# Kernel tuning notes

Measured on AMD Instinct MI355X. Metric: run time of the kernel, lower is better.

## Reference

```python
import jax, jax.numpy as jnp
import numpy as np

B, D_IN, D_DENSE, S1, S2 = 16384, 1024, 1024, 1024, 1024
SPARSITY1, SPARSITY2 = 0.1, 0.01  # fraction of zeros in the 'sparse' weights


def setup_inputs() -> dict:
    key = jax.random.key(0)
    kx, k0, k1, k2, km1, km2 = jax.random.split(key, 6)
    x = jax.random.normal(kx, (B, D_IN), dtype=jnp.float32)
    # dense layer params (nn.Linear): weight [out, in], bias [out]
    w0 = jax.random.normal(k0, (D_DENSE, D_IN), dtype=jnp.float32) / np.sqrt(D_IN)
    b0 = jnp.zeros((D_DENSE,), dtype=jnp.float32)
    # sparse layers: dense randn weight elementwise-masked (mask keeps with prob 1-sparsity)
    w1 = jax.random.normal(k1, (S1, D_DENSE), dtype=jnp.float32)
    mask1 = jax.random.uniform(km1, (S1, D_DENSE)) > SPARSITY1
    b1 = jnp.zeros((S1,), dtype=jnp.float32)
    w2 = jax.random.normal(k2, (S2, S1), dtype=jnp.float32)
    mask2 = jax.random.uniform(km2, (S2, S1)) > SPARSITY2
    b2 = jnp.zeros((S2,), dtype=jnp.float32)
    return {"x": x, "w0": w0, "b0": b0, "w1": w1, "b1": b1, "mask1": mask1,
            "w2": w2, "b2": b2, "mask2": mask2}


def reference(x, w0, b0, w1, b1, mask1, w2, b2, mask2):
    # layer 1: dense linear + ReLU
    h = jax.nn.relu(jnp.einsum('bi,oi->bo', x, w0) + b0)
    # layer 2: masked ('sparse' COO in torch) linear + bias + ReLU
    h = jax.nn.relu(jnp.einsum('bi,oi->bo', h, w1 * mask1) + b1)
    # layer 3: masked linear + bias + ReLU
    out = jax.nn.relu(jnp.einsum('bi,oi->bo', h, w2 * mask2) + b2)
    return out
```

## Files before the change

kernel.cpp:

```cpp
#include <hip/hip_runtime.h>
#include <hip/hip_bf16.h>
#include <cstdint>
#include <cstddef>


typedef __bf16 bf16x8 __attribute__((ext_vector_type(8)));
typedef float  f32x4  __attribute__((ext_vector_type(4)));

#define AS1 __attribute__((address_space(1)))
#define AS3 __attribute__((address_space(3)))

__device__ __forceinline__ void gload_lds16(const void* g, void* l) {
    __builtin_amdgcn_global_load_lds((const AS1 void*)g, (AS3 void*)l, 16, 0, 0);
}

__global__ void detect_mask(const unsigned char* __restrict__ m, int* __restrict__ flag) {
    const int t = threadIdx.x;
    int or1 = 0, or3 = 0;
    for (int e = t; e < 256; e += 64) { or1 |= m[e * 4 + 1]; or3 |= m[e * 4 + 3]; }
    unsigned long long b1 = __ballot(or1 != 0);
    unsigned long long b3 = __ballot(or3 != 0);
    if (t == 0) *flag = b1 ? 1 : (b3 ? 2 : 0);
}

__device__ __forceinline__ void prep_body(const float* __restrict__ w,
                                          const void* __restrict__ mask, int mode,
                                          __bf16* __restrict__ out, long i) {
    float4 a = *reinterpret_cast<const float4*>(w + i);
    float4 b = *reinterpret_cast<const float4*>(w + i + 4);
    float v[8] = {a.x, a.y, a.z, a.w, b.x, b.y, b.z, b.w};
    if (mask) {
        if (mode == 1) {
            const unsigned char* mp = (const unsigned char*)mask;
            #pragma unroll
            for (int j = 0; j < 8; ++j) v[j] = mp[i + j] ? v[j] : 0.f;
        } else if (mode == 0) {
            const int* mp = (const int*)mask;
            #pragma unroll
            for (int j = 0; j < 8; ++j) v[j] = mp[i + j] ? v[j] : 0.f;
        } else {
            const float* mp = (const float*)mask;
            #pragma unroll
            for (int j = 0; j < 8; ++j) v[j] = (mp[i + j] != 0.f) ? v[j] : 0.f;
        }
    }
    bf16x8 o;
    #pragma unroll
    for (int j = 0; j < 8; ++j) o[j] = (__bf16)v[j];
    *reinterpret_cast<bf16x8*>(out + i) = o;
}

__global__ void prep_all(const float* __restrict__ x, __bf16* __restrict__ xb,
                         const float* __restrict__ w0, const float* __restrict__ w1,
                         const float* __restrict__ w2,
                         const void* __restrict__ m1, const void* __restrict__ m2,
                         const int* __restrict__ flag,
                         __bf16* __restrict__ w0b, __bf16* __restrict__ w1b,
                         __bf16* __restrict__ w2b) {
    const int bid = blockIdx.x;
    if (bid < 8192) {
        long i = ((long)bid * blockDim.x + threadIdx.x) * 8;
        float4 a = *reinterpret_cast<const float4*>(x + i);
        float4 b = *reinterpret_cast<const float4*>(x + i + 4);
        bf16x8 o;
        o[0] = (__bf16)a.x; o[1] = (__bf16)a.y; o[2] = (__bf16)a.z; o[3] = (__bf16)a.w;
        o[4] = (__bf16)b.x; o[5] = (__bf16)b.y; o[6] = (__bf16)b.z; o[7] = (__bf16)b.w;
        *reinterpret_cast<bf16x8*>(xb + i) = o;
    } else {
        const int q = bid - 8192, wi = q >> 9, sub = q & 511;
        long i = ((long)sub * blockDim.x + threadIdx.x) * 8;
        const int mode = *flag;
        if (wi == 0)      prep_body(w0, nullptr, mode, w0b, i);
        else if (wi == 1) prep_body(w1, m1,      mode, w1b, i);
        else              prep_body(w2, m2,      mode, w2b, i);
    }
}

__device__ __forceinline__ f32x4 mfma16(bf16x8 a, bf16x8 b, f32x4 c) {
    return __builtin_amdgcn_mfma_f32_16x16x32_bf16(a, b, c, 0, 0, 0);
}

#define MFMAQ(Q, A00, A01, A10, A11)                                        \
    __builtin_amdgcn_s_setprio(1);                                          \
    _Pragma("unroll")                                                       \
    for (int n = 0; n < 4; ++n) {                                           \
        acc[2*(Q)][n]   = mfma16(A00, b[n][0], acc[2*(Q)][n]);              \
        acc[2*(Q)][n]   = mfma16(A01, b[n][1], acc[2*(Q)][n]);              \
        acc[2*(Q)+1][n] = mfma16(A10, b[n][0], acc[2*(Q)+1][n]);            \
        acc[2*(Q)+1][n] = mfma16(A11, b[n][1], acc[2*(Q)+1][n]);            \
    }                                                                       \
    __builtin_amdgcn_s_setprio(0);

#define BAR()   __builtin_amdgcn_s_barrier()
#define LGKM0() asm volatile("s_waitcnt lgkmcnt(0)" ::: "memory")
#define VM8()   asm volatile("s_waitcnt vmcnt(8)" ::: "memory")
#define VM0()   asm volatile("s_waitcnt vmcnt(0)" ::: "memory")

template<bool F32OUT>
__global__ __launch_bounds__(512, 2) void gemm8p(
    const __bf16* __restrict__ A, const __bf16* __restrict__ W,
    const float* __restrict__ bias,
    __bf16* __restrict__ outb, float* __restrict__ outf) {
    constexpr int NT = 16;
    extern __shared__ char smem[];

    const int t   = threadIdx.x;
    const int l   = t & 63, l15 = l & 15, lhi = l >> 4;
    const int w   = t >> 6, wr = w >> 2, wc = w & 3;

    const int bid = blockIdx.x;
    const int swz = (bid & 7) * 32 + (bid >> 3);
    const int bx = swz & 3, by = swz >> 2;
    const int brow = by * 256, bcol = bx * 256;

    const int srow = t >> 3;
    const int scol = (((t & 7) ^ ((t >> 3) & 7)) << 4) >> 1;
    const __bf16* gA = A + (size_t)(brow + srow) * 1024 + scol;
    const __bf16* gW = W + (size_t)(bcol + srow) * 1024 + scol;
    const int woff = (t & 448) * 16;

    char* const ldsA = smem;
    char* const ldsB = smem + 65536;

    auto stageAfull = [&](int d, int k0) {
        const __bf16* g = gA + k0;
        char* p = ldsA + d * 32768 + woff;
        gload_lds16(g,          p);
        gload_lds16(g + 65536,  p + 8192);
        gload_lds16(g + 131072, p + 16384);
        gload_lds16(g + 196608, p + 24576);
    };
    auto stageBh = [&](int d, int h, int k0) {
        const __bf16* g = gW + (size_t)h * 131072 + k0;
        char* p = ldsB + d * 32768 + h * 16384 + woff;
        gload_lds16(g, p);
        gload_lds16(g + 65536, p + 8192);
    };

    const int xorm  = (l & 7) << 4;
    const int koff0 = (lhi * 16) ^ xorm;
    const int koff1 = (64 + lhi * 16) ^ xorm;
    char* const aBase = ldsA + wr * 16384 + l15 * 128;
    char* const bBase = ldsB + wc * 8192 + l15 * 128;

    f32x4 acc[8][4] = {};

    stageAfull(0, 0);  stageBh(0, 0, 0);  stageBh(0, 1, 0);
    stageAfull(1, 64); stageBh(1, 0, 64); stageBh(1, 1, 64);
    VM8(); BAR();

    #pragma unroll 2
    for (int tt = 0; tt < NT; ++tt) {
        const int d  = tt & 1;
        const int k2 = (tt + 2) * 64;
        char* const aB = aBase + d * 32768;
        char* const bB = bBase + d * 32768;
        const bool st = (tt + 2 < NT);

        bf16x8 b[4][2];
        #pragma unroll
        for (int n = 0; n < 4; ++n) {
            b[n][0] = *(const bf16x8*)(bB + n * 2048 + koff0);
            b[n][1] = *(const bf16x8*)(bB + n * 2048 + koff1);
        }
        bf16x8 a00 = *(const bf16x8*)(aB + 0 * 2048 + koff0);
        bf16x8 a01 = *(const bf16x8*)(aB + 0 * 2048 + koff1);
        bf16x8 a10 = *(const bf16x8*)(aB + 1 * 2048 + koff0);
        bf16x8 a11 = *(const bf16x8*)(aB + 1 * 2048 + koff1);
        bf16x8 c00 = *(const bf16x8*)(aB + 2 * 2048 + koff0);
        bf16x8 c01 = *(const bf16x8*)(aB + 2 * 2048 + koff1);
        bf16x8 c10 = *(const bf16x8*)(aB + 3 * 2048 + koff0);
        bf16x8 c11 = *(const bf16x8*)(aB + 3 * 2048 + koff1);
        MFMAQ(0, a00, a01, a10, a11);
        LGKM0(); BAR();

        if (st) stageBh(d, 0, k2);
        a00 = *(const bf16x8*)(aB + 4 * 2048 + koff0);
        a01 = *(const bf16x8*)(aB + 4 * 2048 + koff1);
        a10 = *(const bf16x8*)(aB + 5 * 2048 + koff0);
        a11 = *(const bf16x8*)(aB + 5 * 2048 + koff1);
        MFMAQ(1, c00, c01, c10, c11);
        LGKM0(); BAR();

        if (st) stageBh(d, 1, k2);
        c00 = *(const bf16x8*)(aB + 6 * 2048 + koff0);
        c01 = *(const bf16x8*)(aB + 6 * 2048 + koff1);
        c10 = *(const bf16x8*)(aB + 7 * 2048 + koff0);
        c11 = *(const bf16x8*)(aB + 7 * 2048 + koff1);
        MFMAQ(2, a00, a01, a10, a11);
        LGKM0(); BAR();

        if (st) stageAfull(d, k2);
        MFMAQ(3, c00, c01, c10, c11);
        if (tt <= NT - 3)      { VM8(); BAR(); }
        else if (tt == NT - 2) { VM0(); BAR(); }
    }

    if constexpr (F32OUT) {
        char* const cl = smem;
        #pragma unroll
        for (int chunk = 0; chunk < 2; ++chunk) {
            __syncthreads();
            if (wr == chunk) {
                #pragma unroll
                for (int n = 0; n < 4; ++n) {
                    const int colb = (wc * 64 + n * 16 + l15) * 4;
                    const float bv = bias[bcol + wc * 64 + n * 16 + l15];
                    #pragma unroll
                    for (int m = 0; m < 8; ++m) {
                        #pragma unroll
                        for (int r = 0; r < 4; ++r) {
                            const int row = m * 16 + lhi * 4 + r;
                            float v = acc[m][n][r] + bv;
                            v = v > 0.f ? v : 0.f;
                            *(float*)(cl + row * 1024 + (colb ^ ((row & 12) << 4))) = v;
                        }
                    }
                }
            }
            __syncthreads();
            #pragma unroll
            for (int rd = 0; rd < 16; ++rd) {
                const int off = rd * 8192 + t * 16;
                const int row = off >> 10;
                const int cb  = (off & 1023) ^ ((row & 12) << 4);
                float4 v = *(const float4*)(cl + off);
                *(float4*)((char*)outf +
                           ((size_t)(brow + chunk * 128 + row) * 1024 + bcol) * 4 + cb) = v;
            }
        }
    } else {
        __syncthreads();
        char* const cl = smem;
        #pragma unroll
        for (int n = 0; n < 4; ++n) {
            const int colb = (wc * 64 + n * 16 + l15) * 2;
            const float bv = bias[bcol + wc * 64 + n * 16 + l15];
            #pragma unroll
            for (int m = 0; m < 8; ++m) {
                #pragma unroll
                for (int r = 0; r < 4; ++r) {
                    const int row = wr * 128 + m * 16 + lhi * 4 + r;
                    float v = acc[m][n][r] + bv;
                    v = v > 0.f ? v : 0.f;
                    *(__bf16*)(cl + row * 512 + (colb ^ ((row & 12) << 3))) = (__bf16)v;
                }
            }
        }
        __syncthreads();
        #pragma unroll
        for (int rd = 0; rd < 16; ++rd) {
            const int off = rd * 8192 + t * 16;
            const int row = off >> 9;
            const int cb  = (off & 511) ^ ((row & 12) << 3);
            bf16x8 v = *(const bf16x8*)(cl + off);
            *(bf16x8*)((char*)outb + ((size_t)(brow + row) * 1024 + bcol) * 2 + cb) = v;
        }
    }
}

extern "C" void kernel_launch(void* const* d_in, const int* in_sizes, int n_in,
                              void* d_out, int out_size, void* d_ws, size_t ws_size,
                              hipStream_t stream) {
    const float* x  = (const float*)d_in[0];
    const float* w0 = (const float*)d_in[1];
    const float* b0 = (const float*)d_in[2];
    const float* w1 = (const float*)d_in[3];
    const float* b1 = (const float*)d_in[4];
    const void*  m1 = d_in[5];
    const float* w2 = (const float*)d_in[6];
    const float* b2 = (const float*)d_in[7];
    const void*  m2 = d_in[8];
    float* out = (float*)d_out;

    char* ws = (char*)d_ws;
    __bf16* xb  = (__bf16*)(ws);
    __bf16* h1  = (__bf16*)(ws + (size_t)32 * 1024 * 1024);
    __bf16* w0b = (__bf16*)(ws + (size_t)64 * 1024 * 1024);
    __bf16* w1b = w0b + 1024 * 1024;
    __bf16* w2b = w1b + 1024 * 1024;
    int*   flag = (int*)(w2b + 1024 * 1024);

    hipFuncSetAttribute((const void*)gemm8p<false>,
                        hipFuncAttributeMaxDynamicSharedMemorySize, 131072);
    hipFuncSetAttribute((const void*)gemm8p<true>,
                        hipFuncAttributeMaxDynamicSharedMemorySize, 131072);

    detect_mask<<<1, 64, 0, stream>>>((const unsigned char*)m1, flag);
    prep_all<<<9728, 256, 0, stream>>>(x, xb, w0, w1, w2, m1, m2, flag,
                                       w0b, w1b, w2b);

    gemm8p<false><<<256, 512, 131072, stream>>>(xb, w0b, b0, h1, nullptr);
    gemm8p<false><<<256, 512, 131072, stream>>>(h1, w1b, b1, xb, nullptr);
    gemm8p<true ><<<256, 512, 131072, stream>>>(xb, w2b, b2, nullptr, out);
}
```

Measured before the change: 130.0 us.

## Restructure GEMM main loop into k-half phases with interleaved row mapping

```diff
diff --git a/kernel.cpp b/kernel.cpp
--- a/kernel.cpp
+++ b/kernel.cpp
@@ -80,20 +80,20 @@
     return __builtin_amdgcn_mfma_f32_16x16x32_bf16(a, b, c, 0, 0, 0);
 }
 
-#define MFMAQ(Q, A00, A01, A10, A11)                                        \
+#define MFMAPH(MH, KH)                                                      \
     __builtin_amdgcn_s_setprio(1);                                          \
     _Pragma("unroll")                                                       \
     for (int n = 0; n < 4; ++n) {                                           \
-        acc[2*(Q)][n]   = mfma16(A00, b[n][0], acc[2*(Q)][n]);              \
-        acc[2*(Q)][n]   = mfma16(A01, b[n][1], acc[2*(Q)][n]);              \
-        acc[2*(Q)+1][n] = mfma16(A10, b[n][0], acc[2*(Q)+1][n]);            \
-        acc[2*(Q)+1][n] = mfma16(A11, b[n][1], acc[2*(Q)+1][n]);            \
+        acc[(MH)*4+0][n] = mfma16(a0, b[n][KH], acc[(MH)*4+0][n]);          \
+        acc[(MH)*4+1][n] = mfma16(a1, b[n][KH], acc[(MH)*4+1][n]);          \
+        acc[(MH)*4+2][n] = mfma16(a2, b[n][KH], acc[(MH)*4+2][n]);          \
+        acc[(MH)*4+3][n] = mfma16(a3, b[n][KH], acc[(MH)*4+3][n]);          \
     }                                                                       \
     __builtin_amdgcn_s_setprio(0);
 
-#define BAR()   __builtin_amdgcn_s_barrier()
+#define BAR()   __builtin_amdgcn_s_barrier(); __builtin_amdgcn_sched_barrier(0)
 #define LGKM0() asm volatile("s_waitcnt lgkmcnt(0)" ::: "memory")
-#define VM8()   asm volatile("s_waitcnt vmcnt(8)" ::: "memory")
+#define VM4()   asm volatile("s_waitcnt vmcnt(4)" ::: "memory")
 #define VM0()   asm volatile("s_waitcnt vmcnt(0)" ::: "memory")
 
 template<bool F32OUT>
@@ -122,13 +122,11 @@
     char* const ldsA = smem;
     char* const ldsB = smem + 65536;
 
-    auto stageAfull = [&](int d, int k0) {
-        const __bf16* g = gA + k0;
-        char* p = ldsA + d * 32768 + woff;
-        gload_lds16(g,          p);
-        gload_lds16(g + 65536,  p + 8192);
-        gload_lds16(g + 131072, p + 16384);
-        gload_lds16(g + 196608, p + 24576);
+    auto stageAh = [&](int d, int h, int k0) {
+        const __bf16* g = gA + (size_t)h * 131072 + k0;
+        char* p = ldsA + d * 32768 + h * 16384 + woff;
+        gload_lds16(g, p);
+        gload_lds16(g + 65536, p + 8192);
     };
     auto stageBh = [&](int d, int h, int k0) {
         const __bf16* g = gW + (size_t)h * 131072 + k0;
@@ -140,59 +138,68 @@
     const int xorm  = (l & 7) << 4;
     const int koff0 = (lhi * 16) ^ xorm;
     const int koff1 = (64 + lhi * 16) ^ xorm;
-    char* const aBase = ldsA + wr * 16384 + l15 * 128;
+    char* const aBase = ldsA + (wr * 16 + l15) * 128;
     char* const bBase = ldsB + wc * 8192 + l15 * 128;
 
     f32x4 acc[8][4] = {};
 
-    stageAfull(0, 0);  stageBh(0, 0, 0);  stageBh(0, 1, 0);
-    stageAfull(1, 64); stageBh(1, 0, 64); stageBh(1, 1, 64);
-    VM8(); BAR();
+    stageAh(0, 0, 0);  stageAh(0, 1, 0);
+    stageBh(0, 0, 0);  stageBh(0, 1, 0);
+    stageBh(1, 0, 64); stageBh(1, 1, 64);
+    VM4(); BAR();
 
     #pragma unroll 2
     for (int tt = 0; tt < NT; ++tt) {
         const int d  = tt & 1;
-        const int k2 = (tt + 2) * 64;
+        const int k1 = (tt + 1) * 64, k2 = (tt + 2) * 64;
         char* const aB = aBase + d * 32768;
         char* const bB = bBase + d * 32768;
-        const bool st = (tt + 2 < NT);
-
-        bf16x8 b[4][2];
-        #pragma unroll
-        for (int n = 0; n < 4; ++n) {
-            b[n][0] = *(const bf16x8*)(bB + n * 2048 + koff0);
-            b[n][1] = *(const bf16x8*)(bB + n * 2048 + koff1);
-        }
-        bf16x8 a00 = *(const bf16x8*)(aB + 0 * 2048 + koff0);
-        bf16x8 a01 = *(const bf16x8*)(aB + 0 * 2048 + koff1);
-        bf16x8 a10 = *(const bf16x8*)(aB + 1 * 2048 + koff0);
-        bf16x8 a11 = *(const bf16x8*)(aB + 1 * 2048 + koff1);
-        bf16x8 c00 = *(const bf16x8*)(aB + 2 * 2048 + koff0);
-        bf16x8 c01 = *(const bf16x8*)(aB + 2 * 2048 + koff1);
-        bf16x8 c10 = *(const bf16x8*)(aB + 3 * 2048 + koff0);
-        bf16x8 c11 = *(const bf16x8*)(aB + 3 * 2048 + koff1);
-        MFMAQ(0, a00, a01, a10, a11);
-        LGKM0(); BAR();
-
-        if (st) stageBh(d, 0, k2);
-        a00 = *(const bf16x8*)(aB + 4 * 2048 + koff0);
-        a01 = *(const bf16x8*)(aB + 4 * 2048 + koff1);
-        a10 = *(const bf16x8*)(aB + 5 * 2048 + koff0);
-        a11 = *(const bf16x8*)(aB + 5 * 2048 + koff1);
-        MFMAQ(1, c00, c01, c10, c11);
-        LGKM0(); BAR();
-
-        if (st) stageBh(d, 1, k2);
-        c00 = *(const bf16x8*)(aB + 6 * 2048 + koff0);
-        c01 = *(const bf16x8*)(aB + 6 * 2048 + koff1);
-        c10 = *(const bf16x8*)(aB + 7 * 2048 + koff0);
-        c11 = *(const bf16x8*)(aB + 7 * 2048 + koff1);
-        MFMAQ(2, a00, a01, a10, a11);
-        LGKM0(); BAR();
-
-        if (st) stageAfull(d, k2);
-        MFMAQ(3, c00, c01, c10, c11);
-        if (tt <= NT - 3)      { VM8(); BAR(); }
+        const bool s1 = (tt + 1 < NT), s2 = (tt + 2 < NT);
+        bf16x8 a0, a1, a2, a3, b[4][2];
+
+        a0 = *(const bf16x8*)(aB + 0 * 4096 + koff0);
+        a1 = *(const bf16x8*)(aB + 1 * 4096 + koff0);
+        a2 = *(const bf16x8*)(aB + 2 * 4096 + koff0);
+        a3 = *(const bf16x8*)(aB + 3 * 4096 + koff0);
+        b[0][0] = *(const bf16x8*)(bB + 0 * 2048 + koff0);
+        b[1][0] = *(const bf16x8*)(bB + 1 * 2048 + koff0);
+        b[2][0] = *(const bf16x8*)(bB + 2 * 2048 + koff0);
+        b[3][0] = *(const bf16x8*)(bB + 3 * 2048 + koff0);
+        if (s1) stageAh(d ^ 1, 0, k1);
+        BAR(); LGKM0();
+        MFMAPH(0, 0);
+        BAR();
+
+        a0 = *(const bf16x8*)(aB + 0 * 4096 + koff1);
+        a1 = *(const bf16x8*)(aB + 1 * 4096 + koff1);
+        a2 = *(const bf16x8*)(aB + 2 * 4096 + koff1);
+        a3 = *(const bf16x8*)(aB + 3 * 4096 + koff1);
+        b[0][1] = *(const bf16x8*)(bB + 0 * 2048 + koff1);
+        b[1][1] = *(const bf16x8*)(bB + 1 * 2048 + koff1);
+        b[2][1] = *(const bf16x8*)(bB + 2 * 2048 + koff1);
+        b[3][1] = *(const bf16x8*)(bB + 3 * 2048 + koff1);
+        if (s1) stageAh(d ^ 1, 1, k1);
+        BAR(); LGKM0();
+        MFMAPH(0, 1);
+        BAR();
+
+        a0 = *(const bf16x8*)(aB + 4 * 4096 + koff0);
+        a1 = *(const bf16x8*)(aB + 5 * 4096 + koff0);
+        a2 = *(const bf16x8*)(aB + 6 * 4096 + koff0);
+        a3 = *(const bf16x8*)(aB + 7 * 4096 + koff0);
+        if (s2) stageBh(d, 0, k2);
+        BAR(); LGKM0();
+        MFMAPH(1, 0);
+        BAR();
+
+        a0 = *(const bf16x8*)(aB + 4 * 4096 + koff1);
+        a1 = *(const bf16x8*)(aB + 5 * 4096 + koff1);
+        a2 = *(const bf16x8*)(aB + 6 * 4096 + koff1);
+        a3 = *(const bf16x8*)(aB + 7 * 4096 + koff1);
+        if (s2) stageBh(d, 1, k2);
+        BAR(); LGKM0();
+        MFMAPH(1, 1);
+        if (tt < NT - 2)       { VM4(); BAR(); }
         else if (tt == NT - 2) { VM0(); BAR(); }
     }
 
@@ -201,20 +208,18 @@
         #pragma unroll
         for (int chunk = 0; chunk < 2; ++chunk) {
             __syncthreads();
-            if (wr == chunk) {
+            #pragma unroll
+            for (int n = 0; n < 4; ++n) {
+                const int colb = (wc * 64 + n * 16 + l15) * 4;
+                const float bv = bias[bcol + wc * 64 + n * 16 + l15];
                 #pragma unroll
-                for (int n = 0; n < 4; ++n) {
-                    const int colb = (wc * 64 + n * 16 + l15) * 4;
-                    const float bv = bias[bcol + wc * 64 + n * 16 + l15];
+                for (int mm = 0; mm < 4; ++mm) {
                     #pragma unroll
-                    for (int m = 0; m < 8; ++m) {
-                        #pragma unroll
-                        for (int r = 0; r < 4; ++r) {
-                            const int row = m * 16 + lhi * 4 + r;
-                            float v = acc[m][n][r] + bv;
-                            v = v > 0.f ? v : 0.f;
-                            *(float*)(cl + row * 1024 + (colb ^ ((row & 12) << 4))) = v;
-                        }
+                    for (int r = 0; r < 4; ++r) {
+                        const int row = mm * 32 + wr * 16 + lhi * 4 + r;
+                        float v = acc[chunk * 4 + mm][n] [r] + bv;
+                        v = v > 0.f ? v : 0.f;
+                        *(float*)(cl + row * 1024 + (colb ^ ((row & 12) << 4))) = v;
                     }
                 }
             }
@@ -240,7 +245,7 @@
             for (int m = 0; m < 8; ++m) {
                 #pragma unroll
                 for (int r = 0; r < 4; ++r) {
-                    const int row = wr * 128 + m * 16 + lhi * 4 + r;
+                    const int row = m * 32 + wr * 16 + lhi * 4 + r;
                     float v = acc[m][n][r] + bv;
                     v = v > 0.f ? v : 0.f;
                     *(__bf16*)(cl + row * 512 + (colb ^ ((row & 12) << 3))) = (__bf16)v;
```

Result: no change. 132.3 us (+1.8%).

## Shrink GEMM tiles to 128x128 with 4-wave blocks for higher occupancy

Applied to the files above, without the earlier changes.

```diff
diff --git a/kernel.cpp b/kernel.cpp
--- a/kernel.cpp
+++ b/kernel.cpp
@@ -80,24 +80,22 @@
     return __builtin_amdgcn_mfma_f32_16x16x32_bf16(a, b, c, 0, 0, 0);
 }
 
-#define MFMAQ(Q, A00, A01, A10, A11)                                        \
+#define MFMAR(M, A0, A1)                                                    \
     __builtin_amdgcn_s_setprio(1);                                          \
     _Pragma("unroll")                                                       \
     for (int n = 0; n < 4; ++n) {                                           \
-        acc[2*(Q)][n]   = mfma16(A00, b[n][0], acc[2*(Q)][n]);              \
-        acc[2*(Q)][n]   = mfma16(A01, b[n][1], acc[2*(Q)][n]);              \
-        acc[2*(Q)+1][n] = mfma16(A10, b[n][0], acc[2*(Q)+1][n]);            \
-        acc[2*(Q)+1][n] = mfma16(A11, b[n][1], acc[2*(Q)+1][n]);            \
+        acc[M][n] = mfma16(A0, b[n][0], acc[M][n]);                         \
+        acc[M][n] = mfma16(A1, b[n][1], acc[M][n]);                         \
     }                                                                       \
     __builtin_amdgcn_s_setprio(0);
 
-#define BAR()   __builtin_amdgcn_s_barrier()
+#define BAR()   __builtin_amdgcn_s_barrier(); __builtin_amdgcn_sched_barrier(0)
 #define LGKM0() asm volatile("s_waitcnt lgkmcnt(0)" ::: "memory")
 #define VM8()   asm volatile("s_waitcnt vmcnt(8)" ::: "memory")
 #define VM0()   asm volatile("s_waitcnt vmcnt(0)" ::: "memory")
 
 template<bool F32OUT>
-__global__ __launch_bounds__(512, 2) void gemm8p(
+__global__ __launch_bounds__(256, 2) void gemm8p(
     const __bf16* __restrict__ A, const __bf16* __restrict__ W,
     const float* __restrict__ bias,
     __bf16* __restrict__ outb, float* __restrict__ outf) {
@@ -106,44 +104,44 @@
 
     const int t   = threadIdx.x;
     const int l   = t & 63, l15 = l & 15, lhi = l >> 4;
-    const int w   = t >> 6, wr = w >> 2, wc = w & 3;
+    const int w   = t >> 6, wr = w >> 1, wc = w & 1;
 
     const int bid = blockIdx.x;
-    const int swz = (bid & 7) * 32 + (bid >> 3);
-    const int bx = swz & 3, by = swz >> 2;
-    const int brow = by * 256, bcol = bx * 256;
+    const int swz = (bid & 7) * 128 + (bid >> 3);
+    const int bx = swz & 7, by = swz >> 3;
+    const int brow = by * 128, bcol = bx * 128;
 
     const int srow = t >> 3;
     const int scol = (((t & 7) ^ ((t >> 3) & 7)) << 4) >> 1;
     const __bf16* gA = A + (size_t)(brow + srow) * 1024 + scol;
     const __bf16* gW = W + (size_t)(bcol + srow) * 1024 + scol;
-    const int woff = (t & 448) * 16;
+    const int woff = (t & 192) * 16;
 
     char* const ldsA = smem;
-    char* const ldsB = smem + 65536;
+    char* const ldsB = smem + 32768;
 
     auto stageAfull = [&](int d, int k0) {
         const __bf16* g = gA + k0;
-        char* p = ldsA + d * 32768 + woff;
-        gload_lds16(g,          p);
-        gload_lds16(g + 65536,  p + 8192);
-        gload_lds16(g + 131072, p + 16384);
-        gload_lds16(g + 196608, p + 24576);
+        char* p = ldsA + d * 16384 + woff;
+        gload_lds16(g,         p);
+        gload_lds16(g + 32768, p + 4096);
+        gload_lds16(g + 65536, p + 8192);
+        gload_lds16(g + 98304, p + 12288);
     };
     auto stageBh = [&](int d, int h, int k0) {
-        const __bf16* g = gW + (size_t)h * 131072 + k0;
-        char* p = ldsB + d * 32768 + h * 16384 + woff;
+        const __bf16* g = gW + (size_t)h * 65536 + k0;
+        char* p = ldsB + d * 16384 + h * 8192 + woff;
         gload_lds16(g, p);
-        gload_lds16(g + 65536, p + 8192);
+        gload_lds16(g + 32768, p + 4096);
     };
 
     const int xorm  = (l & 7) << 4;
     const int koff0 = (lhi * 16) ^ xorm;
     const int koff1 = (64 + lhi * 16) ^ xorm;
-    char* const aBase = ldsA + wr * 16384 + l15 * 128;
-    char* const bBase = ldsB + wc * 8192 + l15 * 128;
-
-    f32x4 acc[8][4] = {};
+    char* const aBase = ldsA + (wr * 64 + l15) * 128;
+    char* const bBase = ldsB + (wc * 64 + l15) * 128;
+
+    f32x4 acc[4][4] = {};
 
     stageAfull(0, 0);  stageBh(0, 0, 0);  stageBh(0, 1, 0);
     stageAfull(1, 64); stageBh(1, 0, 64); stageBh(1, 1, 64);
@@ -153,8 +151,8 @@
     for (int tt = 0; tt < NT; ++tt) {
         const int d  = tt & 1;
         const int k2 = (tt + 2) * 64;
-        char* const aB = aBase + d * 32768;
-        char* const bB = bBase + d * 32768;
+        char* const aB = aBase + d * 16384;
+        char* const bB = bBase + d * 16384;
         const bool st = (tt + 2 < NT);
 
         bf16x8 b[4][2];
@@ -163,71 +161,57 @@
             b[n][0] = *(const bf16x8*)(bB + n * 2048 + koff0);
             b[n][1] = *(const bf16x8*)(bB + n * 2048 + koff1);
         }
-        bf16x8 a00 = *(const bf16x8*)(aB + 0 * 2048 + koff0);
-        bf16x8 a01 = *(const bf16x8*)(aB + 0 * 2048 + koff1);
-        bf16x8 a10 = *(const bf16x8*)(aB + 1 * 2048 + koff0);
-        bf16x8 a11 = *(const bf16x8*)(aB + 1 * 2048 + koff1);
-        bf16x8 c00 = *(const bf16x8*)(aB + 2 * 2048 + koff0);
-        bf16x8 c01 = *(const bf16x8*)(aB + 2 * 2048 + koff1);
-        bf16x8 c10 = *(const bf16x8*)(aB + 3 * 2048 + koff0);
-        bf16x8 c11 = *(const bf16x8*)(aB + 3 * 2048 + koff1);
-        MFMAQ(0, a00, a01, a10, a11);
+        bf16x8 a0 = *(const bf16x8*)(aB + 0 * 2048 + koff0);
+        bf16x8 a1 = *(const bf16x8*)(aB + 0 * 2048 + koff1);
+        bf16x8 c0 = *(const bf16x8*)(aB + 1 * 2048 + koff0);
+        bf16x8 c1 = *(const bf16x8*)(aB + 1 * 2048 + koff1);
+        MFMAR(0, a0, a1);
         LGKM0(); BAR();
 
         if (st) stageBh(d, 0, k2);
-        a00 = *(const bf16x8*)(aB + 4 * 2048 + koff0);
-        a01 = *(const bf16x8*)(aB + 4 * 2048 + koff1);
-        a10 = *(const bf16x8*)(aB + 5 * 2048 + koff0);
-        a11 = *(const bf16x8*)(aB + 5 * 2048 + koff1);
-        MFMAQ(1, c00, c01, c10, c11);
+        a0 = *(const bf16x8*)(aB + 2 * 2048 + koff0);
+        a1 = *(const bf16x8*)(aB + 2 * 2048 + koff1);
+        MFMAR(1, c0, c1);
         LGKM0(); BAR();
 
         if (st) stageBh(d, 1, k2);
-        c00 = *(const bf16x8*)(aB + 6 * 2048 + koff0);
-        c01 = *(const bf16x8*)(aB + 6 * 2048 + koff1);
-        c10 = *(const bf16x8*)(aB + 7 * 2048 + koff0);
-        c11 = *(const bf16x8*)(aB + 7 * 2048 + koff1);
-        MFMAQ(2, a00, a01, a10, a11);
+        c0 = *(const bf16x8*)(aB + 3 * 2048 + koff0);
+        c1 = *(const bf16x8*)(aB + 3 * 2048 + koff1);
+        MFMAR(2, a0, a1);
         LGKM0(); BAR();
 
         if (st) stageAfull(d, k2);
-        MFMAQ(3, c00, c01, c10, c11);
+        MFMAR(3, c0, c1);
         if (tt <= NT - 3)      { VM8(); BAR(); }
         else if (tt == NT - 2) { VM0(); BAR(); }
     }
 
     if constexpr (F32OUT) {
+        __syncthreads();
         char* const cl = smem;
         #pragma unroll
-        for (int chunk = 0; chunk < 2; ++chunk) {
-            __syncthreads();
-            if (wr == chunk) {
+        for (int n = 0; n < 4; ++n) {
+            const int colb = (wc * 64 + n * 16 + l15) * 4;
+            const float bv = bias[bcol + wc * 64 + n * 16 + l15];
+            #pragma unroll
+            for (int m = 0; m < 4; ++m) {
                 #pragma unroll
-                for (int n = 0; n < 4; ++n) {
-                    const int colb = (wc * 64 + n * 16 + l15) * 4;
-                    const float bv = bias[bcol + wc * 64 + n * 16 + l15];
-                    #pragma unroll
-                    for (int m = 0; m < 8; ++m) {
-                        #pragma unroll
-                        for (int r = 0; r < 4; ++r) {
-                            const int row = m * 16 + lhi * 4 + r;
-                            float v = acc[m][n][r] + bv;
-                            v = v > 0.f ? v : 0.f;
-                            *(float*)(cl + row * 1024 + (colb ^ ((row & 12) << 4))) = v;
-                        }
-                    }
+                for (int r = 0; r < 4; ++r) {
+                    const int row = wr * 64 + m * 16 + lhi * 4 + r;
+                    float v = acc[m][n][r] + bv;
+                    v = v > 0.f ? v : 0.f;
+                    *(float*)(cl + row * 512 + (colb ^ ((row & 12) << 4))) = v;
                 }
             }
-            __syncthreads();
-            #pragma unroll
-            for (int rd = 0; rd < 16; ++rd) {
-                const int off = rd * 8192 + t * 16;
-                const int row = off >> 10;
-                const int cb  = (off & 1023) ^ ((row & 12) << 4);
-                float4 v = *(const float4*)(cl + off);
-                *(float4*)((char*)outf +
-                           ((size_t)(brow + chunk * 128 + row) * 1024 + bcol) * 4 + cb) = v;
-            }
+        }
+        __syncthreads();
+        #pragma unroll
+        for (int rd = 0; rd < 16; ++rd) {
+            const int off = rd * 4096 + t * 16;
+            const int row = off >> 9;
+            const int cb  = (off & 511) ^ ((row & 12) << 4);
+            float4 v = *(const float4*)(cl + off);
+            *(float4*)((char*)outf + ((size_t)(brow + row) * 1024 + bcol) * 4 + cb) = v;
         }
     } else {
         __syncthreads();
@@ -237,22 +221,22 @@
             const int colb = (wc * 64 + n * 16 + l15) * 2;
             const float bv = bias[bcol + wc * 64 + n * 16 + l15];
             #pragma unroll
-            for (int m = 0; m < 8; ++m) {
+            for (int m = 0; m < 4; ++m) {
                 #pragma unroll
                 for (int r = 0; r < 4; ++r) {
-                    const int row = wr * 128 + m * 16 + lhi * 4 + r;
+                    const int row = wr * 64 + m * 16 + lhi * 4 + r;
                     float v = acc[m][n][r] + bv;
                     v = v > 0.f ? v : 0.f;
-                    *(__bf16*)(cl + row * 512 + (colb ^ ((row & 12) << 3))) = (__bf16)v;
+                    *(__bf16*)(cl + row * 256 + (colb ^ ((row & 12) << 3))) = (__bf16)v;
                 }
             }
         }
         __syncthreads();
         #pragma unroll
-        for (int rd = 0; rd < 16; ++rd) {
-            const int off = rd * 8192 + t * 16;
-            const int row = off >> 9;
-            const int cb  = (off & 511) ^ ((row & 12) << 3);
+        for (int rd = 0; rd < 8; ++rd) {
+            const int off = rd * 4096 + t * 16;
+            const int row = off >> 8;
+            const int cb  = (off & 255) ^ ((row & 12) << 3);
             bf16x8 v = *(const bf16x8*)(cl + off);
             *(bf16x8*)((char*)outb + ((size_t)(brow + row) * 1024 + bcol) * 2 + cb) = v;
         }
@@ -282,15 +266,15 @@
     int*   flag = (int*)(w2b + 1024 * 1024);
 
     hipFuncSetAttribute((const void*)gemm8p<false>,
-                        hipFuncAttributeMaxDynamicSharedMemorySize, 131072);
+                        hipFuncAttributeMaxDynamicSharedMemorySize, 65536);
     hipFuncSetAttribute((const void*)gemm8p<true>,
-                        hipFuncAttributeMaxDynamicSharedMemorySize, 131072);
+                        hipFuncAttributeMaxDynamicSharedMemorySize, 65536);
 
     detect_mask<<<1, 64, 0, stream>>>((const unsigned char*)m1, flag);
     prep_all<<<9728, 256, 0, stream>>>(x, xb, w0, w1, w2, m1, m2, flag,
                                        w0b, w1b, w2b);
 
-    gemm8p<false><<<256, 512, 131072, stream>>>(xb, w0b, b0, h1, nullptr);
-    gemm8p<false><<<256, 512, 131072, stream>>>(h1, w1b, b1, xb, nullptr);
-    gemm8p<true ><<<256, 512, 131072, stream>>>(xb, w2b, b2, nullptr, out);
-}
+    gemm8p<false><<<1024, 256, 65536, stream>>>(xb, w0b, b0, h1, nullptr);
+    gemm8p<false><<<1024, 256, 65536, stream>>>(h1, w1b, b1, xb, nullptr);
+    gemm8p<true ><<<1024, 256, 65536, stream>>>(xb, w2b, b2, nullptr, out);
+}
```

Measured after the change: 139.8 us. 7.6% more time.

## Switch GEMM to 32x32x16 MFMA tiles and fold mask detection into prep

Applied to the files above, without the earlier changes.

```diff
diff --git a/kernel.cpp b/kernel.cpp
--- a/kernel.cpp
+++ b/kernel.cpp
@@ -5,22 +5,13 @@
 
 
 typedef __bf16 bf16x8 __attribute__((ext_vector_type(8)));
-typedef float  f32x4  __attribute__((ext_vector_type(4)));
+typedef float  f32x16 __attribute__((ext_vector_type(16)));
 
 #define AS1 __attribute__((address_space(1)))
 #define AS3 __attribute__((address_space(3)))
 
 __device__ __forceinline__ void gload_lds16(const void* g, void* l) {
     __builtin_amdgcn_global_load_lds((const AS1 void*)g, (AS3 void*)l, 16, 0, 0);
-}
-
-__global__ void detect_mask(const unsigned char* __restrict__ m, int* __restrict__ flag) {
-    const int t = threadIdx.x;
-    int or1 = 0, or3 = 0;
-    for (int e = t; e < 256; e += 64) { or1 |= m[e * 4 + 1]; or3 |= m[e * 4 + 3]; }
-    unsigned long long b1 = __ballot(or1 != 0);
-    unsigned long long b3 = __ballot(or3 != 0);
-    if (t == 0) *flag = b1 ? 1 : (b3 ? 2 : 0);
 }
 
 __device__ __forceinline__ void prep_body(const float* __restrict__ w,
@@ -54,12 +45,12 @@
                          const float* __restrict__ w0, const float* __restrict__ w1,
                          const float* __restrict__ w2,
                          const void* __restrict__ m1, const void* __restrict__ m2,
-                         const int* __restrict__ flag,
                          __bf16* __restrict__ w0b, __bf16* __restrict__ w1b,
                          __bf16* __restrict__ w2b) {
     const int bid = blockIdx.x;
+    const int t   = threadIdx.x;
     if (bid < 8192) {
-        long i = ((long)bid * blockDim.x + threadIdx.x) * 8;
+        long i = ((long)bid * blockDim.x + t) * 8;
         float4 a = *reinterpret_cast<const float4*>(x + i);
         float4 b = *reinterpret_cast<const float4*>(x + i + 4);
         bf16x8 o;
@@ -67,31 +58,39 @@
         o[4] = (__bf16)b.x; o[5] = (__bf16)b.y; o[6] = (__bf16)b.z; o[7] = (__bf16)b.w;
         *reinterpret_cast<bf16x8*>(xb + i) = o;
     } else {
+        __shared__ int smode;
+        if (t < 64) {
+            const unsigned char* mm = (const unsigned char*)m1;
+            int or1 = 0, or3 = 0;
+            for (int e = t; e < 256; e += 64) { or1 |= mm[e * 4 + 1]; or3 |= mm[e * 4 + 3]; }
+            unsigned long long b1 = __ballot(or1 != 0);
+            unsigned long long b3 = __ballot(or3 != 0);
+            if (t == 0) smode = b1 ? 1 : (b3 ? 2 : 0);
+        }
+        __syncthreads();
+        const int mode = smode;
         const int q = bid - 8192, wi = q >> 9, sub = q & 511;
-        long i = ((long)sub * blockDim.x + threadIdx.x) * 8;
-        const int mode = *flag;
+        long i = ((long)sub * blockDim.x + t) * 8;
         if (wi == 0)      prep_body(w0, nullptr, mode, w0b, i);
         else if (wi == 1) prep_body(w1, m1,      mode, w1b, i);
         else              prep_body(w2, m2,      mode, w2b, i);
     }
 }
 
-__device__ __forceinline__ f32x4 mfma16(bf16x8 a, bf16x8 b, f32x4 c) {
-    return __builtin_amdgcn_mfma_f32_16x16x32_bf16(a, b, c, 0, 0, 0);
-}
-
-#define MFMAQ(Q, A00, A01, A10, A11)                                        \
+__device__ __forceinline__ f32x16 mfma32(bf16x8 a, bf16x8 b, f32x16 c) {
+    return __builtin_amdgcn_mfma_f32_32x32x16_bf16(a, b, c, 0, 0, 0);
+}
+
+#define MFMAG(MT, A)                                                        \
     __builtin_amdgcn_s_setprio(1);                                          \
     _Pragma("unroll")                                                       \
-    for (int n = 0; n < 4; ++n) {                                           \
-        acc[2*(Q)][n]   = mfma16(A00, b[n][0], acc[2*(Q)][n]);              \
-        acc[2*(Q)][n]   = mfma16(A01, b[n][1], acc[2*(Q)][n]);              \
-        acc[2*(Q)+1][n] = mfma16(A10, b[n][0], acc[2*(Q)+1][n]);            \
-        acc[2*(Q)+1][n] = mfma16(A11, b[n][1], acc[2*(Q)+1][n]);            \
+    for (int kc = 0; kc < 4; ++kc) {                                        \
+        acc[MT][0] = mfma32(A[kc], b[0][kc], acc[MT][0]);                   \
+        acc[MT][1] = mfma32(A[kc], b[1][kc], acc[MT][1]);                   \
     }                                                                       \
     __builtin_amdgcn_s_setprio(0);
 
-#define BAR()   __builtin_amdgcn_s_barrier()
+#define BAR()   __builtin_amdgcn_s_barrier(); __builtin_amdgcn_sched_barrier(0)
 #define LGKM0() asm volatile("s_waitcnt lgkmcnt(0)" ::: "memory")
 #define VM8()   asm volatile("s_waitcnt vmcnt(8)" ::: "memory")
 #define VM0()   asm volatile("s_waitcnt vmcnt(0)" ::: "memory")
@@ -104,9 +103,9 @@
     constexpr int NT = 16;
     extern __shared__ char smem[];
 
-    const int t   = threadIdx.x;
-    const int l   = t & 63, l15 = l & 15, lhi = l >> 4;
-    const int w   = t >> 6, wr = w >> 2, wc = w & 3;
+    const int t    = threadIdx.x;
+    const int l    = t & 63, l31 = l & 31, lhi5 = l >> 5;
+    const int w    = t >> 6, wr = w >> 2, wc = w & 3;
 
     const int bid = blockIdx.x;
     const int swz = (bid & 7) * 32 + (bid >> 3);
@@ -137,13 +136,14 @@
         gload_lds16(g + 65536, p + 8192);
     };
 
-    const int xorm  = (l & 7) << 4;
-    const int koff0 = (lhi * 16) ^ xorm;
-    const int koff1 = (64 + lhi * 16) ^ xorm;
-    char* const aBase = ldsA + wr * 16384 + l15 * 128;
-    char* const bBase = ldsB + wc * 8192 + l15 * 128;
-
-    f32x4 acc[8][4] = {};
+    const int xorm = (l & 7) << 4;
+    int koff[4];
+    #pragma unroll
+    for (int kc = 0; kc < 4; ++kc) koff[kc] = (kc * 32 + lhi5 * 16) ^ xorm;
+    char* const aBase = ldsA + (wr * 128 + l31) * 128;
+    char* const bBase = ldsB + (wc * 64 + l31) * 128;
+
+    f32x16 acc[4][2] = {};
 
     stageAfull(0, 0);  stageBh(0, 0, 0);  stageBh(0, 1, 0);
     stageAfull(1, 64); stageBh(1, 0, 64); stageBh(1, 1, 64);
@@ -157,41 +157,36 @@
         char* const bB = bBase + d * 32768;
         const bool st = (tt + 2 < NT);
 
-        bf16x8 b[4][2];
-        #pragma unroll
-        for (int n = 0; n < 4; ++n) {
-            b[n][0] = *(const bf16x8*)(bB + n * 2048 + koff0);
-            b[n][1] = *(const bf16x8*)(bB + n * 2048 + koff1);
-        }
-        bf16x8 a00 = *(const bf16x8*)(aB + 0 * 2048 + koff0);
-        bf16x8 a01 = *(const bf16x8*)(aB + 0 * 2048 + koff1);
-        bf16x8 a10 = *(const bf16x8*)(aB + 1 * 2048 + koff0);
-        bf16x8 a11 = *(const bf16x8*)(aB + 1 * 2048 + koff1);
-        bf16x8 c00 = *(const bf16x8*)(aB + 2 * 2048 + koff0);
-        bf16x8 c01 = *(const bf16x8*)(aB + 2 * 2048 + koff1);
-        bf16x8 c10 = *(const bf16x8*)(aB + 3 * 2048 + koff0);
-        bf16x8 c11 = *(const bf16x8*)(aB + 3 * 2048 + koff1);
-        MFMAQ(0, a00, a01, a10, a11);
+        bf16x8 b[2][4], a[4], c[4];
+        #pragma unroll
+        for (int kc = 0; kc < 4; ++kc) {
+            b[0][kc] = *(const bf16x8*)(bB + 0 * 4096 + koff[kc]);
+            b[1][kc] = *(const bf16x8*)(bB + 1 * 4096 + koff[kc]);
+        }
+        #pragma unroll
+        for (int kc = 0; kc < 4; ++kc) {
+            a[kc] = *(const bf16x8*)(aB + 0 * 4096 + koff[kc]);
+            c[kc] = *(const bf16x8*)(aB + 1 * 4096 + koff[kc]);
+        }
+        MFMAG(0, a);
         LGKM0(); BAR();
 
         if (st) stageBh(d, 0, k2);
-        a00 = *(const bf16x8*)(aB + 4 * 2048 + koff0);
-        a01 = *(const bf16x8*)(aB + 4 * 2048 + koff1);
-        a10 = *(const bf16x8*)(aB + 5 * 2048 + koff0);
-        a11 = *(const bf16x8*)(aB + 5 * 2048 + koff1);
-        MFMAQ(1, c00, c01, c10, c11);
+        #pragma unroll
+        for (int kc = 0; kc < 4; ++kc)
+            a[kc] = *(const bf16x8*)(aB + 2 * 4096 + koff[kc]);
+        MFMAG(1, c);
         LGKM0(); BAR();
 
         if (st) stageBh(d, 1, k2);
-        c00 = *(const bf16x8*)(aB + 6 * 2048 + koff0);
-        c01 = *(const bf16x8*)(aB + 6 * 2048 + koff1);
-        c10 = *(const bf16x8*)(aB + 7 * 2048 + koff0);
-        c11 = *(const bf16x8*)(aB + 7 * 2048 + koff1);
-        MFMAQ(2, a00, a01, a10, a11);
+        #pragma unroll
+        for (int kc = 0; kc < 4; ++kc)
+            c[kc] = *(const bf16x8*)(aB + 3 * 4096 + koff[kc]);
+        MFMAG(2, a);
         LGKM0(); BAR();
 
         if (st) stageAfull(d, k2);
-        MFMAQ(3, c00, c01, c10, c11);
+        MFMAG(3, c);
         if (tt <= NT - 3)      { VM8(); BAR(); }
         else if (tt == NT - 2) { VM0(); BAR(); }
     }
@@ -203,15 +198,16 @@
             __syncthreads();
             if (wr == chunk) {
                 #pragma unroll
-                for (int n = 0; n < 4; ++n) {
-                    const int colb = (wc * 64 + n * 16 + l15) * 4;
-                    const float bv = bias[bcol + wc * 64 + n * 16 + l15];
+                for (int nt = 0; nt < 2; ++nt) {
+                    const int col = wc * 64 + nt * 32 + l31;
+                    const int colb = col * 4;
+                    const float bv = bias[bcol + col];
                     #pragma unroll
-                    for (int m = 0; m < 8; ++m) {
+                    for (int mt = 0; mt < 4; ++mt) {
                         #pragma unroll
-                        for (int r = 0; r < 4; ++r) {
-                            const int row = m * 16 + lhi * 4 + r;
-                            float v = acc[m][n][r] + bv;
+                        for (int r = 0; r < 16; ++r) {
+                            const int row = mt * 32 + (r & 3) + 8 * (r >> 2) + 4 * lhi5;
+                            float v = acc[mt][nt][r] + bv;
                             v = v > 0.f ? v : 0.f;
                             *(float*)(cl + row * 1024 + (colb ^ ((row & 12) << 4))) = v;
                         }
@@ -233,15 +229,16 @@
         __syncthreads();
         char* const cl = smem;
         #pragma unroll
-        for (int n = 0; n < 4; ++n) {
-            const int colb = (wc * 64 + n * 16 + l15) * 2;
-            const float bv = bias[bcol + wc * 64 + n * 16 + l15];
-            #pragma unroll
-            for (int m = 0; m < 8; ++m) {
+        for (int nt = 0; nt < 2; ++nt) {
+            const int col = wc * 64 + nt * 32 + l31;
+            const int colb = col * 2;
+            const float bv = bias[bcol + col];
+            #pragma unroll
+            for (int mt = 0; mt < 4; ++mt) {
                 #pragma unroll
-                for (int r = 0; r < 4; ++r) {
-                    const int row = wr * 128 + m * 16 + lhi * 4 + r;
-                    float v = acc[m][n][r] + bv;
+                for (int r = 0; r < 16; ++r) {
+                    const int row = wr * 128 + mt * 32 + (r & 3) + 8 * (r >> 2) + 4 * lhi5;
+                    float v = acc[mt][nt][r] + bv;
                     v = v > 0.f ? v : 0.f;
                     *(__bf16*)(cl + row * 512 + (colb ^ ((row & 12) << 3))) = (__bf16)v;
                 }
@@ -279,15 +276,13 @@
     __bf16* w0b = (__bf16*)(ws + (size_t)64 * 1024 * 1024);
     __bf16* w1b = w0b + 1024 * 1024;
     __bf16* w2b = w1b + 1024 * 1024;
-    int*   flag = (int*)(w2b + 1024 * 1024);
 
     hipFuncSetAttribute((const void*)gemm8p<false>,
                         hipFuncAttributeMaxDynamicSharedMemorySize, 131072);
     hipFuncSetAttribute((const void*)gemm8p<true>,
                         hipFuncAttributeMaxDynamicSharedMemorySize, 131072);
 
-    detect_mask<<<1, 64, 0, stream>>>((const unsigned char*)m1, flag);
-    prep_all<<<9728, 256, 0, stream>>>(x, xb, w0, w1, w2, m1, m2, flag,
+    prep_all<<<9728, 256, 0, stream>>>(x, xb, w0, w1, w2, m1, m2,
                                        w0b, w1b, w2b);
 
     gemm8p<false><<<256, 512, 131072, stream>>>(xb, w0b, b0, h1, nullptr);
```

Result: slower. 139.7 us (+7.5%).
